# Kernel optimization log

Hardware: AMD Instinct MI355X
Metric: run time of the kernel (lower is better)

## Reference

```python
import jax, jax.numpy as jnp
import numpy as np

TEMP = 0.5  # matches temperature init kwarg
EPS = 1e-12  # F.normalize eps


def _l2norm(x):
    # F.normalize(x, dim=1): x / max(||x||, eps)
    n = jnp.linalg.norm(x, axis=1, keepdims=True)
    return x / jnp.maximum(n, EPS)


def setup_inputs() -> dict:
    key = jax.random.key(0)
    k1, k2 = jax.random.split(key)
    B, D = 4096, 256
    return {
        "x_i": jax.random.normal(k1, (B, D), dtype=jnp.float32),
        "x_j": jax.random.normal(k2, (B, D), dtype=jnp.float32),
    }


def reference(x_i, x_j):
    B = x_i.shape[0]
    z = jnp.concatenate([_l2norm(x_i), _l2norm(x_j)], axis=0)  # [2B, D]
    # cosine similarity of normalized rows == matmul (avoids NxNxD broadcast)
    sim = (z @ z.T) / TEMP  # [2B, 2B]
    idx = jnp.arange(B)
    # diagonals at offsets +B and -B = positive pairs
    pos = jnp.concatenate([sim[idx, idx + B], sim[idx + B, idx]])  # [2B]
    exp_sim = jnp.exp(sim)
    # neg = all off-diagonal entries per row (neg_mask = ~eye(2B))
    exp_neg = exp_sim.sum(axis=1) - jnp.exp(jnp.diagonal(sim))  # [2B]
    exp_pos = jnp.exp(pos)
    loss = -jnp.log(exp_pos / (exp_pos + exp_neg))
    return loss.mean()
```

## Files before the change

kernel.cpp:

```cpp
#include <hip/hip_runtime.h>
#include <hip/hip_bf16.h>

typedef __attribute__((ext_vector_type(8))) int   i32x8;
typedef __attribute__((ext_vector_type(4))) int   i32x4;
typedef __attribute__((ext_vector_type(4))) float f32x4;

constexpr int BB = 4096;
constexpr int D  = 256;
constexpr int R2 = 8192;
constexpr int NSPLIT = 32;
constexpr int CPB = R2 / NSPLIT;
constexpr int NG  = CPB / 16;
constexpr float SCALE = 1.6986436005760381f;
constexpr float E2 = 7.38905609893065f;

__device__ __forceinline__ void async16(const unsigned char* g, unsigned char* l) {
    __builtin_amdgcn_global_load_lds(
        (const __attribute__((address_space(1))) void*)g,
        (__attribute__((address_space(3))) void*)l,
        16, 0, 0);
}

#define MFMA8(A, B, C) \
    __builtin_amdgcn_mfma_scale_f32_16x16x128_f8f6f4((A), (B), (C), 0, 0, 0, 127, 0, 127)

__global__ __launch_bounds__(256) void norm_kernel(const float* __restrict__ xi,
                                                   const float* __restrict__ xj,
                                                   int* __restrict__ z8,
                                                   float* __restrict__ pos,
                                                   float* __restrict__ out) {
    const int wid = threadIdx.x >> 6, lane = threadIdx.x & 63;
    const int k = blockIdx.x * 4 + wid;
    if (blockIdx.x == 0 && threadIdx.x == 0) out[0] = 0.f;
    const float4* a4 = reinterpret_cast<const float4*>(xi + (size_t)k * D);
    const float4* b4 = reinterpret_cast<const float4*>(xj + (size_t)k * D);
    float4 a = a4[lane], b = b4[lane];
    float ssi = a.x*a.x + a.y*a.y + a.z*a.z + a.w*a.w;
    float ssj = b.x*b.x + b.y*b.y + b.z*b.z + b.w*b.w;
    float dot = a.x*b.x + a.y*b.y + a.z*b.z + a.w*b.w;
#pragma unroll
    for (int off = 32; off; off >>= 1) {
        ssi += __shfl_xor(ssi, off);
        ssj += __shfl_xor(ssj, off);
        dot += __shfl_xor(dot, off);
    }
    const float inv_i = 1.0f / fmaxf(sqrtf(ssi), 1e-12f);
    const float inv_j = 1.0f / fmaxf(sqrtf(ssj), 1e-12f);
    const float si = inv_i * SCALE, sj = inv_j * SCALE;
    int pi = __builtin_amdgcn_cvt_pk_fp8_f32(a.x*si, a.y*si, 0, false);
    pi     = __builtin_amdgcn_cvt_pk_fp8_f32(a.z*si, a.w*si, pi, true);
    int pj = __builtin_amdgcn_cvt_pk_fp8_f32(b.x*sj, b.y*sj, 0, false);
    pj     = __builtin_amdgcn_cvt_pk_fp8_f32(b.z*sj, b.w*sj, pj, true);
    z8[(size_t)k * 64 + lane]        = pi;
    z8[(size_t)(k + BB) * 64 + lane] = pj;
    if (lane == 0) pos[k] = dot * inv_i * inv_j * 2.0f;
}

__global__ __launch_bounds__(512, 4) void sim_kernel(const unsigned char* __restrict__ z8,
                                                     float* __restrict__ partial) {
    __shared__ unsigned char tb[CPB * D];
    const int tid = threadIdx.x;
    const int wid = tid >> 6, lane = tid & 63;
    const int lrow = lane & 15, quad = lane >> 4;
    const int r0 = blockIdx.x * 256 + wid * 32;
    const int cbase = blockIdx.y * CPB;

    {
        const int srcg = (tid & 15) ^ ((tid >> 4) & 15);
        const unsigned char* gs = z8 + (size_t)(cbase + (tid >> 4)) * D + srcg * 16;
        unsigned char* ds = tb + tid * 16;
#pragma unroll
        for (int i = 0; i < 8; ++i)
            async16(gs + (size_t)i * 32 * D, ds + i * 8192);
    }

    const unsigned char* abase = z8 + (size_t)(r0 + lrow) * D + quad * 32;
    i32x8 a0k0 = *reinterpret_cast<const i32x8*>(abase             );
    i32x8 a0k1 = *reinterpret_cast<const i32x8*>(abase        + 128);
    i32x8 a1k0 = *reinterpret_cast<const i32x8*>(abase + 16*D      );
    i32x8 a1k1 = *reinterpret_cast<const i32x8*>(abase + 16*D + 128);
    asm volatile("" : "+v"(a0k0), "+v"(a0k1), "+v"(a1k0), "+v"(a1k1));

    f32x4 racc0 = {0.f,0.f,0.f,0.f}, racc1 = {0.f,0.f,0.f,0.f};

    __syncthreads();

    const int pe0 = (quad * 2) ^ lrow;
    const int pe1 = (8 + quad * 2) ^ lrow;
    const unsigned char* rbp = tb + lrow * D;
#pragma unroll 4
    for (int n = 0; n < NG; ++n) {
        const i32x4 lo0 = *reinterpret_cast<const i32x4*>(rbp + pe0*16);
        const i32x4 hi0 = *reinterpret_cast<const i32x4*>(rbp + (pe0^1)*16);
        const i32x4 lo1 = *reinterpret_cast<const i32x4*>(rbp + pe1*16);
        const i32x4 hi1 = *reinterpret_cast<const i32x4*>(rbp + (pe1^1)*16);
        rbp += 16 * D;
        const i32x8 b0 = __builtin_shufflevector(lo0, hi0, 0,1,2,3,4,5,6,7);
        const i32x8 b1 = __builtin_shufflevector(lo1, hi1, 0,1,2,3,4,5,6,7);

        f32x4 c0 = {0.f,0.f,0.f,0.f}, c1 = {0.f,0.f,0.f,0.f};
        c0 = MFMA8(a0k0, b0, c0);  c0 = MFMA8(a0k1, b1, c0);
        c1 = MFMA8(a1k0, b0, c1);  c1 = MFMA8(a1k1, b1, c1);

        racc0[0] += __builtin_amdgcn_exp2f(c0[0]);
        racc0[1] += __builtin_amdgcn_exp2f(c0[1]);
        racc0[2] += __builtin_amdgcn_exp2f(c0[2]);
        racc0[3] += __builtin_amdgcn_exp2f(c0[3]);
        racc1[0] += __builtin_amdgcn_exp2f(c1[0]);
        racc1[1] += __builtin_amdgcn_exp2f(c1[1]);
        racc1[2] += __builtin_amdgcn_exp2f(c1[2]);
        racc1[3] += __builtin_amdgcn_exp2f(c1[3]);
    }

#define REDUCE_STORE(RV, M)                                                     \
    {                                                                           \
        _Pragma("unroll")                                                       \
        for (int j = 0; j < 4; ++j) {                                           \
            float v = (RV)[j];                                                  \
            v += __shfl_xor(v, 1);                                              \
            v += __shfl_xor(v, 2);                                              \
            v += __shfl_xor(v, 4);                                              \
            v += __shfl_xor(v, 8);                                              \
            if (lrow == 0)                                                      \
                partial[(size_t)blockIdx.y * R2 + r0 + (M)*16 + quad*4 + j] = v;\
        }                                                                       \
    }
    REDUCE_STORE(racc0, 0)
    REDUCE_STORE(racc1, 1)
#undef REDUCE_STORE
}

__global__ __launch_bounds__(256) void reduce_kernel(const float* __restrict__ partial,
                                                     const float* __restrict__ pos,
                                                     float* __restrict__ out) {
    __shared__ float wsum[4];
    const int tid = threadIdx.x;
    const int r = blockIdx.x * 256 + tid;
    float S = 0.f;
#pragma unroll
    for (int s = 0; s < NSPLIT; ++s) S += partial[(size_t)s * R2 + r];
    const float p = pos[r & (BB - 1)];
    float lsum = __logf(__expf(p) + S - E2) - p;
#pragma unroll
    for (int off = 32; off; off >>= 1) lsum += __shfl_xor(lsum, off);
    if ((tid & 63) == 0) wsum[tid >> 6] = lsum;
    __syncthreads();
    if (tid == 0) {
        float t = wsum[0] + wsum[1] + wsum[2] + wsum[3];
        atomicAdd(out, t * (1.0f / (float)R2));
    }
}

extern "C" void kernel_launch(void* const* d_in, const int* in_sizes, int n_in,
                              void* d_out, int out_size, void* d_ws, size_t ws_size,
                              hipStream_t stream) {
    (void)in_sizes; (void)n_in; (void)out_size; (void)ws_size;
    const float* xi = (const float*)d_in[0];
    const float* xj = (const float*)d_in[1];
    float* out = (float*)d_out;

    unsigned char* z8 = (unsigned char*)d_ws;
    float* partial = (float*)((char*)d_ws + (size_t)R2 * D);
    float* pos     = (float*)((char*)d_ws + (size_t)R2 * D + (size_t)NSPLIT*R2*4);

    norm_kernel<<<BB / 4, 256, 0, stream>>>(xi, xj, (int*)z8, pos, out);
    sim_kernel<<<dim3(R2 / 256, NSPLIT), 512, 0, stream>>>(z8, partial);
    reduce_kernel<<<R2 / 256, 256, 0, stream>>>(partial, pos, out);
}
```

Baseline: 83.74 us.

## Exploit symmetry of similarity matrix by computing only upper-triangular tiles

The sim kernel now launches only the upper-triangular block tiles of the 8192x8192 similarity matrix, since z·zᵀ is symmetric. Each tile accumulates row sums as before and also accumulates column sums through shared-memory atomics, writing them as the transposed tile's partial. This roughly halves the MFMA and exp work. In exchange it adds an LDS atomic per iteration, an extra barrier, a serial loop to map block index to tile, and uneven diagonal-tile work.

```diff
diff --git a/kernel.cpp b/kernel.cpp
--- a/kernel.cpp
+++ b/kernel.cpp
@@ -11,6 +11,7 @@
 constexpr int NSPLIT = 32;
 constexpr int CPB = R2 / NSPLIT;
 constexpr int NG  = CPB / 16;
+constexpr int NTRI = NSPLIT * (NSPLIT + 1) / 2;
 constexpr float SCALE = 1.6986436005760381f;
 constexpr float E2 = 7.38905609893065f;
 
@@ -59,11 +60,19 @@
 __global__ __launch_bounds__(512, 4) void sim_kernel(const unsigned char* __restrict__ z8,
                                                      float* __restrict__ partial) {
     __shared__ unsigned char tb[CPB * D];
+    __shared__ float colacc[CPB];
     const int tid = threadIdx.x;
     const int wid = tid >> 6, lane = tid & 63;
     const int lrow = lane & 15, quad = lane >> 4;
-    const int r0 = blockIdx.x * 256 + wid * 32;
-    const int cbase = blockIdx.y * CPB;
+
+    int t = blockIdx.x, bx = 0;
+    while (t >= (NSPLIT - bx)) { t -= (NSPLIT - bx); ++bx; }
+    const int by = bx + t;
+
+    const int r0 = bx * 256 + wid * 32;
+    const int cbase = by * CPB;
+
+    if (tid < CPB) colacc[tid] = 0.f;
 
     {
         const int srcg = (tid & 15) ^ ((tid >> 4) & 15);
@@ -102,14 +111,19 @@
         c0 = MFMA8(a0k0, b0, c0);  c0 = MFMA8(a0k1, b1, c0);
         c1 = MFMA8(a1k0, b0, c1);  c1 = MFMA8(a1k1, b1, c1);
 
-        racc0[0] += __builtin_amdgcn_exp2f(c0[0]);
-        racc0[1] += __builtin_amdgcn_exp2f(c0[1]);
-        racc0[2] += __builtin_amdgcn_exp2f(c0[2]);
-        racc0[3] += __builtin_amdgcn_exp2f(c0[3]);
-        racc1[0] += __builtin_amdgcn_exp2f(c1[0]);
-        racc1[1] += __builtin_amdgcn_exp2f(c1[1]);
-        racc1[2] += __builtin_amdgcn_exp2f(c1[2]);
-        racc1[3] += __builtin_amdgcn_exp2f(c1[3]);
+        const float e0 = __builtin_amdgcn_exp2f(c0[0]);
+        const float e1 = __builtin_amdgcn_exp2f(c0[1]);
+        const float e2 = __builtin_amdgcn_exp2f(c0[2]);
+        const float e3 = __builtin_amdgcn_exp2f(c0[3]);
+        const float e4 = __builtin_amdgcn_exp2f(c1[0]);
+        const float e5 = __builtin_amdgcn_exp2f(c1[1]);
+        const float e6 = __builtin_amdgcn_exp2f(c1[2]);
+        const float e7 = __builtin_amdgcn_exp2f(c1[3]);
+        racc0[0] += e0;  racc0[1] += e1;  racc0[2] += e2;  racc0[3] += e3;
+        racc1[0] += e4;  racc1[1] += e5;  racc1[2] += e6;  racc1[3] += e7;
+
+        const float cs = ((e0 + e1) + (e2 + e3)) + ((e4 + e5) + (e6 + e7));
+        atomicAdd(&colacc[n * 16 + lrow], cs);
     }
 
 #define REDUCE_STORE(RV, M)                                                     \
@@ -122,12 +136,16 @@
             v += __shfl_xor(v, 4);                                              \
             v += __shfl_xor(v, 8);                                              \
             if (lrow == 0)                                                      \
-                partial[(size_t)blockIdx.y * R2 + r0 + (M)*16 + quad*4 + j] = v;\
+                partial[(size_t)by * R2 + r0 + (M)*16 + quad*4 + j] = v;        \
         }                                                                       \
     }
     REDUCE_STORE(racc0, 0)
     REDUCE_STORE(racc1, 1)
 #undef REDUCE_STORE
+
+    __syncthreads();
+    if (bx != by && tid < CPB)
+        partial[(size_t)bx * R2 + cbase + tid] = colacc[tid];
 }
 
 __global__ __launch_bounds__(256) void reduce_kernel(const float* __restrict__ partial,
@@ -164,6 +182,6 @@
     float* pos     = (float*)((char*)d_ws + (size_t)R2 * D + (size_t)NSPLIT*R2*4);
 
     norm_kernel<<<BB / 4, 256, 0, stream>>>(xi, xj, (int*)z8, pos, out);
-    sim_kernel<<<dim3(R2 / 256, NSPLIT), 512, 0, stream>>>(z8, partial);
+    sim_kernel<<<NTRI, 512, 0, stream>>>(z8, partial);
     reduce_kernel<<<R2 / 256, 256, 0, stream>>>(partial, pos, out);
 }
```

After: 110.7 us. +32.2%, slower.
